# Kernel tuning notes

Hardware: AMD Instinct MI355X
Metric: run time of the kernel (lower is better)

The kernel has to match this reference:

```python
import jax, jax.numpy as jnp
import numpy as np

B, N, T, F = 4, 5000, 16, 64
E = 80000
H, C_OUT = 4, 16           # attention heads, per-head out channels
S = H * C_OUT              # stream_dim = 64
HID = 192                  # encoder hidden_dim = 3 * S
NEG_SLOPE = 0.2
EPS_SM = 1e-16             # PyG softmax eps
EPS_LN = 1e-5


def setup_inputs() -> dict:
    key = jax.random.key(0)
    ks = jax.random.split(key, 12)
    rn = lambda k, shape, s=0.1: jax.random.normal(k, shape, jnp.float32) * s
    return {
        "x_seq": rn(ks[0], (T, B, N, F), 1.0),
        "lin_w": rn(ks[1], (3, S, F)),          # per-stream GAT linear [out,in]
        "att_src": rn(ks[2], (3, H, C_OUT)),
        "att_dst": rn(ks[3], (3, H, C_OUT)),
        "gat_bias": jnp.zeros((3, S), jnp.float32),
        "w_ih": rn(ks[4], (3, 4 * S, S)),       # LSTMCell input weights (i,f,g,o)
        "w_hh": rn(ks[5], (3, 4 * S, S)),
        "b_ih": jnp.zeros((3, 4 * S), jnp.float32),
        "b_hh": jnp.zeros((3, 4 * S), jnp.float32),
        "ln_g": jnp.ones((3, S), jnp.float32),
        "ln_b": jnp.zeros((3, S), jnp.float32),
        "attn_w1": rn(ks[6], (HID // 2, 3 * S)),
        "attn_b1": jnp.zeros((HID // 2,), jnp.float32),
        "attn_w2": rn(ks[7], (3, HID // 2)),
        "attn_b2": jnp.zeros((3,), jnp.float32),
        "edge_index": jax.random.randint(ks[8], (2, E), 0, N, jnp.int32),
    }


def _batched_edges(edge_index):
    # replicate the graph B times with node-id offsets, then add self loops
    offs = (jnp.arange(B, dtype=edge_index.dtype) * N)[:, None]
    src = (edge_index[0][None, :] + offs).reshape(-1)
    dst = (edge_index[1][None, :] + offs).reshape(-1)
    loops = jnp.arange(B * N, dtype=edge_index.dtype)
    return jnp.concatenate([src, loops]), jnp.concatenate([dst, loops])


def _gat(x, src, dst, lin_w, a_src, a_dst, bias):
    # x: [B,N,F] -> out: [B,N,S]
    xt = (x.reshape(B * N, F) @ lin_w.T).reshape(B * N, H, C_OUT)
    xj, xi = xt[src], xt[dst]                               # [Eb,H,C]
    a = jnp.einsum('ehc,hc->eh', xj, a_src) + jnp.einsum('ehc,hc->eh', xi, a_dst)
    a = jax.nn.leaky_relu(a, NEG_SLOPE)
    amax = jax.ops.segment_max(a, dst, num_segments=B * N)  # segment-softmax over target
    ex = jnp.exp(a - amax[dst])
    den = jax.ops.segment_sum(ex, dst, num_segments=B * N)
    alpha = ex / (den[dst] + EPS_SM)
    out = jax.ops.segment_sum(xj * alpha[..., None], dst, num_segments=B * N)
    return out.reshape(B, N, S) + bias


def _cell(x, h, c, src, dst, lin_w, a_s, a_d, gb, wih, whh, bih, bhh, g, b):
    # one TemporalGNNCell step; h,c: [B*N,S]
    sp = _gat(x, src, dst, lin_w, a_s, a_d, gb).reshape(B * N, S)
    gates = sp @ wih.T + bih + h @ whh.T + bhh
    i, f, gg, o = jnp.split(gates, 4, axis=-1)
    c_new = jax.nn.sigmoid(f) * c + jax.nn.sigmoid(i) * jnp.tanh(gg)
    h_new = jax.nn.sigmoid(o) * jnp.tanh(c_new)
    mu = h_new.mean(-1, keepdims=True)
    var = ((h_new - mu) ** 2).mean(-1, keepdims=True)
    h_ln = (h_new - mu) / jnp.sqrt(var + EPS_LN) * g + b
    return h_ln, c_new


def reference(x_seq, lin_w, att_src, att_dst, gat_bias, w_ih, w_hh, b_ih, b_hh,
              ln_g, ln_b, attn_w1, attn_b1, attn_w2, attn_b2, edge_index):
    src, dst = _batched_edges(edge_index)
    z = jnp.zeros((B * N, S), x_seq.dtype)
    hf = cf = hm = cm = hs = cs = z
    outs = []
    for t in range(T):
        x_t = x_seq[t]
        hf, cf = _cell(x_t, hf, cf, src, dst, lin_w[0], att_src[0], att_dst[0], gat_bias[0],
                       w_ih[0], w_hh[0], b_ih[0], b_hh[0], ln_g[0], ln_b[0])
        if t % 15 == 0:
            hm, cm = _cell(x_t, hm, cm, src, dst, lin_w[1], att_src[1], att_dst[1], gat_bias[1],
                           w_ih[1], w_hh[1], b_ih[1], b_hh[1], ln_g[1], ln_b[1])
        if t % 150 == 0:
            hs, cs = _cell(x_t, hs, cs, src, dst, lin_w[2], att_src[2], att_dst[2], gat_bias[2],
                           w_ih[2], w_hh[2], b_ih[2], b_hh[2], ln_g[2], ln_b[2])
        fast, med, slow = hf, hm, hs
        ms = jnp.concatenate([fast, med, slow], axis=-1)       # [B*N, 3S]
        w = jax.nn.softmax(jax.nn.relu(ms @ attn_w1.T + attn_b1) @ attn_w2.T + attn_b2, axis=-1)
        outs.append(w[:, 0:1] * fast + w[:, 1:2] * med + w[:, 2:3] * slow)
    # stack(dim=1) then permute(0,2,1,3): [B, N, T, S]
    out = jnp.stack(outs, 0).reshape(T, B, N, S).transpose(1, 2, 0, 3)
    return out
```

## Files before the change

### kernel.cpp

```cpp
#include <hip/hip_runtime.h>
#include <cstddef>

#define NNODES 20000
#define TT 16
#define EE 80000
#define BE 320000
#define EB 340000
#define NPER 5000

__device__ __forceinline__ float sigf(float x) { return 1.0f / (1.0f + __expf(-x)); }
__device__ __forceinline__ float lreluf(float x) { return x > 0.0f ? x : 0.2f * x; }

__global__ __launch_bounds__(256) void deg_count_k(const int* __restrict__ eidx, int* __restrict__ deg) {
  int e = blockIdx.x * 256 + threadIdx.x;
  if (e >= EB) return;
  int dst;
  if (e < BE) { int r = e % EE; int b = e / EE; dst = eidx[EE + r] + b * NPER; }
  else dst = e - BE;
  atomicAdd(&deg[dst], 1);
}

__global__ __launch_bounds__(1024) void scan_k(const int* __restrict__ deg, int* __restrict__ startp) {
  __shared__ int buf[1024];
  __shared__ int carry_s;
  int tid = threadIdx.x;
  if (tid == 0) carry_s = 0;
  __syncthreads();
  for (int base = 0; base < NNODES; base += 1024) {
    int i = base + tid;
    int v = (i < NNODES) ? deg[i] : 0;
    buf[tid] = v;
    __syncthreads();
    for (int off = 1; off < 1024; off <<= 1) {
      int tv = (tid >= off) ? buf[tid - off] : 0;
      __syncthreads();
      buf[tid] += tv;
      __syncthreads();
    }
    int incl = buf[tid];
    int carry = carry_s;
    if (i < NNODES) startp[i] = carry + incl - v;
    __syncthreads();
    if (tid == 1023) carry_s = carry + incl;
    __syncthreads();
  }
  if (tid == 0) startp[NNODES] = carry_s;
}

__global__ __launch_bounds__(256) void fill_k(const int* __restrict__ eidx, const int* __restrict__ startp,
                                              int* __restrict__ cnt, int* __restrict__ adj) {
  int e = blockIdx.x * 256 + threadIdx.x;
  if (e >= EB) return;
  int src, dst;
  if (e < BE) { int r = e % EE; int b = e / EE; src = eidx[r] + b * NPER; dst = eidx[EE + r] + b * NPER; }
  else { src = e - BE; dst = src; }
  int p = atomicAdd(&cnt[dst], 1);
  adj[startp[dst] + p] = src;
}

__global__ __launch_bounds__(256) void gemm_k64(
    const float* __restrict__ A0, const float* __restrict__ A1, const float* __restrict__ A2,
    const float* __restrict__ W0, const float* __restrict__ W1, const float* __restrict__ W2,
    int wld, int nseg, int M, int N,
    const float* __restrict__ bias0, const float* __restrict__ bias1,
    int relu, float* __restrict__ C, int cld,
    const float* __restrict__ attS, const float* __restrict__ attD,
    float* __restrict__ asrcOut, float* __restrict__ adstOut)
{
  __shared__ float As[16][132];
  __shared__ float Bs[16][68];
  const int tid = threadIdx.x;
  const int m0 = blockIdx.x * 128;
  const int n0 = blockIdx.y * 64;
  const int tr = tid >> 4;
  const int tc = tid & 15;
  float acc[8][4];
#pragma unroll
  for (int r = 0; r < 8; ++r)
#pragma unroll
    for (int c = 0; c < 4; ++c) acc[r][c] = 0.0f;

  const int lk = (tid & 3) * 4;
  const int lm = tid >> 2;

  for (int seg = 0; seg < nseg; ++seg) {
    const float* Ap = (seg == 0) ? A0 : ((seg == 1) ? A1 : A2);
    const float* Wp = (seg == 0) ? W0 : ((seg == 1) ? W1 : W2);
    for (int ko = 0; ko < 64; ko += 16) {
#pragma unroll
      for (int i = 0; i < 2; ++i) {
        int m = lm + i * 64;
        int gm = m0 + m;
        float4 v = make_float4(0.f, 0.f, 0.f, 0.f);
        if (gm < M) v = *reinterpret_cast<const float4*>(Ap + (size_t)gm * 64 + ko + lk);
        As[lk + 0][m] = v.x; As[lk + 1][m] = v.y; As[lk + 2][m] = v.z; As[lk + 3][m] = v.w;
      }
      {
        int gn = n0 + lm;
        float4 v = make_float4(0.f, 0.f, 0.f, 0.f);
        if (gn < N) v = *reinterpret_cast<const float4*>(Wp + (size_t)gn * wld + ko + lk);
        Bs[lk + 0][lm] = v.x; Bs[lk + 1][lm] = v.y; Bs[lk + 2][lm] = v.z; Bs[lk + 3][lm] = v.w;
      }
      __syncthreads();
#pragma unroll
      for (int k = 0; k < 16; ++k) {
        float4 a0 = *reinterpret_cast<const float4*>(&As[k][tr * 8]);
        float4 a1 = *reinterpret_cast<const float4*>(&As[k][tr * 8 + 4]);
        float4 bb = *reinterpret_cast<const float4*>(&Bs[k][tc * 4]);
        float av[8] = {a0.x, a0.y, a0.z, a0.w, a1.x, a1.y, a1.z, a1.w};
        float bv[4] = {bb.x, bb.y, bb.z, bb.w};
#pragma unroll
        for (int r = 0; r < 8; ++r)
#pragma unroll
          for (int c = 0; c < 4; ++c)
            acc[r][c] = fmaf(av[r], bv[c], acc[r][c]);
      }
      __syncthreads();
    }
  }

#pragma unroll
  for (int r = 0; r < 8; ++r) {
    int gm = m0 + tr * 8 + r;
    if (gm < M) {
#pragma unroll
      for (int c = 0; c < 4; ++c) {
        int gn = n0 + tc * 4 + c;
        if (gn < N) {
          float v = acc[r][c];
          if (bias0) v += bias0[gn];
          if (bias1) v += bias1[gn];
          if (relu) v = fmaxf(v, 0.0f);
          C[(size_t)gm * cld + gn] = v;
          acc[r][c] = v;
        }
      }
    }
  }

  if (attS != nullptr) {
    int g = tc >> 2;
    float s0 = attS[tc * 4 + 0], s1 = attS[tc * 4 + 1], s2 = attS[tc * 4 + 2], s3 = attS[tc * 4 + 3];
    float d0 = attD[tc * 4 + 0], d1 = attD[tc * 4 + 1], d2 = attD[tc * 4 + 2], d3 = attD[tc * 4 + 3];
#pragma unroll
    for (int r = 0; r < 8; ++r) {
      float ps = acc[r][0] * s0 + acc[r][1] * s1 + acc[r][2] * s2 + acc[r][3] * s3;
      float pd = acc[r][0] * d0 + acc[r][1] * d1 + acc[r][2] * d2 + acc[r][3] * d3;
      ps += __shfl_xor(ps, 1); ps += __shfl_xor(ps, 2);
      pd += __shfl_xor(pd, 1); pd += __shfl_xor(pd, 2);
      int gm = m0 + tr * 8 + r;
      if ((tc & 3) == 0 && gm < M) {
        asrcOut[gm * 4 + g] = ps;
        adstOut[gm * 4 + g] = pd;
      }
    }
  }
}

__global__ __launch_bounds__(256) void edge_gather_k(
    const int* __restrict__ startp, const int* __restrict__ adj,
    const float* __restrict__ asrc, const float* __restrict__ adst,
    const float* __restrict__ xt, const float* __restrict__ bias,
    float* __restrict__ sp)
{
  int node = blockIdx.x * 4 + (threadIdx.x >> 6);
  if (node >= NNODES) return;
  int lane = threadIdx.x & 63;
  int s0 = startp[node];
  int deg = startp[node + 1] - s0;

  float4 adv = *reinterpret_cast<const float4*>(adst + (size_t)node * 4);
  float ad0 = adv.x, ad1 = adv.y, ad2 = adv.z, ad3 = adv.w;

  float mx0 = -1e30f, mx1 = -1e30f, mx2 = -1e30f, mx3 = -1e30f;
  for (int e = lane; e < deg; e += 64) {
    int src = adj[s0 + e];
    float4 av = *reinterpret_cast<const float4*>(asrc + (size_t)src * 4);
    mx0 = fmaxf(mx0, lreluf(av.x + ad0));
    mx1 = fmaxf(mx1, lreluf(av.y + ad1));
    mx2 = fmaxf(mx2, lreluf(av.z + ad2));
    mx3 = fmaxf(mx3, lreluf(av.w + ad3));
  }
#pragma unroll
  for (int off = 1; off < 64; off <<= 1) {
    mx0 = fmaxf(mx0, __shfl_xor(mx0, off));
    mx1 = fmaxf(mx1, __shfl_xor(mx1, off));
    mx2 = fmaxf(mx2, __shfl_xor(mx2, off));
    mx3 = fmaxf(mx3, __shfl_xor(mx3, off));
  }
  float dn0 = 0.f, dn1 = 0.f, dn2 = 0.f, dn3 = 0.f;
  for (int e = lane; e < deg; e += 64) {
    int src = adj[s0 + e];
    float4 av = *reinterpret_cast<const float4*>(asrc + (size_t)src * 4);
    dn0 += __expf(lreluf(av.x + ad0) - mx0);
    dn1 += __expf(lreluf(av.y + ad1) - mx1);
    dn2 += __expf(lreluf(av.z + ad2) - mx2);
    dn3 += __expf(lreluf(av.w + ad3) - mx3);
  }
#pragma unroll
  for (int off = 1; off < 64; off <<= 1) {
    dn0 += __shfl_xor(dn0, off);
    dn1 += __shfl_xor(dn1, off);
    dn2 += __shfl_xor(dn2, off);
    dn3 += __shfl_xor(dn3, off);
  }
  int h = lane >> 4;
  float mxh = (h == 0) ? mx0 : (h == 1) ? mx1 : (h == 2) ? mx2 : mx3;
  float adh = (h == 0) ? ad0 : (h == 1) ? ad1 : (h == 2) ? ad2 : ad3;
  float dnh = (h == 0) ? dn0 : (h == 1) ? dn1 : (h == 2) ? dn2 : dn3;
  float rdh = 1.0f / (dnh + 1e-16f);

  float accv = 0.0f;
  for (int e = 0; e < deg; ++e) {
    int src = adj[s0 + e];
    float a = lreluf(asrc[src * 4 + h] + adh);
    float alpha = __expf(a - mxh) * rdh;
    accv = fmaf(alpha, xt[(size_t)src * 64 + lane], accv);
  }
  sp[(size_t)node * 64 + lane] = accv + bias[lane];
}

__global__ __launch_bounds__(256) void lstm_update_k(
    const float* __restrict__ gates, float* __restrict__ cst, float* __restrict__ hst,
    const float* __restrict__ g_ln, const float* __restrict__ b_ln)
{
  int node = blockIdx.x * 4 + (threadIdx.x >> 6);
  if (node >= NNODES) return;
  int lane = threadIdx.x & 63;
  size_t gb = (size_t)node * 256;
  float gi = gates[gb + lane];
  float gf = gates[gb + 64 + lane];
  float gg = gates[gb + 128 + lane];
  float go = gates[gb + 192 + lane];
  float c = cst[(size_t)node * 64 + lane];
  float cn = sigf(gf) * c + sigf(gi) * tanhf(gg);
  float hn = sigf(go) * tanhf(cn);

  float s = hn;
#pragma unroll
  for (int off = 1; off < 64; off <<= 1) s += __shfl_xor(s, off);
  float mu = s * (1.0f / 64.0f);
  float d = hn - mu;
  float v = d * d;
#pragma unroll
  for (int off = 1; off < 64; off <<= 1) v += __shfl_xor(v, off);
  float var = v * (1.0f / 64.0f);
  float hl = d * rsqrtf(var + 1e-5f) * g_ln[lane] + b_ln[lane];
  hst[(size_t)node * 64 + lane] = hl;
  cst[(size_t)node * 64 + lane] = cn;
}

__global__ __launch_bounds__(256) void mix_final_k(
    const float* __restrict__ hidden, const float* __restrict__ w2, const float* __restrict__ b2,
    const float* __restrict__ hf, const float* __restrict__ hm, const float* __restrict__ hs,
    float* __restrict__ out, int t)
{
  int node = blockIdx.x * 4 + (threadIdx.x >> 6);
  if (node >= NNODES) return;
  int lane = threadIdx.x & 63;
  size_t hb = (size_t)node * 96;
  float h0 = hidden[hb + lane];
  int j2 = 64 + (lane & 31);
  float h1 = hidden[hb + j2];
  if (lane >= 32) h1 = 0.0f;

  float p0 = w2[lane] * h0 + w2[j2] * h1;
  float p1 = w2[96 + lane] * h0 + w2[96 + j2] * h1;
  float p2 = w2[192 + lane] * h0 + w2[192 + j2] * h1;
#pragma unroll
  for (int off = 1; off < 64; off <<= 1) {
    p0 += __shfl_xor(p0, off);
    p1 += __shfl_xor(p1, off);
    p2 += __shfl_xor(p2, off);
  }
  float l0 = p0 + b2[0], l1 = p1 + b2[1], l2 = p2 + b2[2];
  float m = fmaxf(l0, fmaxf(l1, l2));
  float e0 = __expf(l0 - m), e1 = __expf(l1 - m), e2 = __expf(l2 - m);
  float rs = 1.0f / (e0 + e1 + e2);
  float w0 = e0 * rs, w1v = e1 * rs, w2v = e2 * rs;

  size_t nb = (size_t)node * 64 + lane;
  float o = w0 * hf[nb] + w1v * hm[nb] + w2v * hs[nb];
  out[((size_t)node * TT + t) * 64 + lane] = o;
}

static inline void run_cell(hipStream_t stream, int c,
    const float* xtp, float* hstate, float* cstate,
    const float* lin_w, const float* att_src, const float* att_dst, const float* gat_bias,
    const float* w_ih, const float* w_hh, const float* b_ih, const float* b_hh,
    const float* ln_g, const float* ln_b,
    float* xt, float* sp, float* gates, float* asrc, float* adst,
    const int* startp, const int* adj)
{
  gemm_k64<<<dim3(157, 1), 256, 0, stream>>>(
      xtp, nullptr, nullptr, lin_w + c * 4096, nullptr, nullptr, 64, 1, NNODES, 64,
      nullptr, nullptr, 0, xt, 64, att_src + c * 64, att_dst + c * 64, asrc, adst);
  edge_gather_k<<<5000, 256, 0, stream>>>(startp, adj, asrc, adst, xt, gat_bias + c * 64, sp);
  gemm_k64<<<dim3(157, 4), 256, 0, stream>>>(
      sp, hstate, nullptr, w_ih + c * 16384, w_hh + c * 16384, nullptr, 64, 2, NNODES, 256,
      b_ih + c * 256, b_hh + c * 256, 0, gates, 256, nullptr, nullptr, nullptr, nullptr);
  lstm_update_k<<<5000, 256, 0, stream>>>(gates, cstate, hstate, ln_g + c * 64, ln_b + c * 64);
}

extern "C" void kernel_launch(void* const* d_in, const int* in_sizes, int n_in,
                              void* d_out, int out_size, void* d_ws, size_t ws_size,
                              hipStream_t stream) {
  const float* x_seq   = (const float*)d_in[0];
  const float* lin_w   = (const float*)d_in[1];
  const float* att_src = (const float*)d_in[2];
  const float* att_dst = (const float*)d_in[3];
  const float* gat_bias= (const float*)d_in[4];
  const float* w_ih    = (const float*)d_in[5];
  const float* w_hh    = (const float*)d_in[6];
  const float* b_ih    = (const float*)d_in[7];
  const float* b_hh    = (const float*)d_in[8];
  const float* ln_g    = (const float*)d_in[9];
  const float* ln_b    = (const float*)d_in[10];
  const float* w1      = (const float*)d_in[11];
  const float* b1      = (const float*)d_in[12];
  const float* w2      = (const float*)d_in[13];
  const float* b2      = (const float*)d_in[14];
  const int*   eidx    = (const int*)d_in[15];
  float* out = (float*)d_out;

  float* fbase = (float*)d_ws;
  float* xt     = fbase;
  float* sp     = xt + 1280000;
  float* gates  = sp + 1280000;
  float* hidden = gates + 5120000;
  float* asrc   = hidden + 1920000;
  float* adst   = asrc + 80000;
  float* hf = adst + 80000;
  float* cf = hf + 1280000;
  float* hm = cf + 1280000;
  float* cm = hm + 1280000;
  float* hs = cm + 1280000;
  float* cs = hs + 1280000;
  int* deg    = (int*)(cs + 1280000);
  int* cnt    = deg + 20000;
  int* startp = cnt + 20000;
  int* adj    = startp + 20001;

  hipMemsetAsync(hf, 0, (size_t)6 * 1280000 * sizeof(float), stream);
  hipMemsetAsync(deg, 0, (size_t)40000 * sizeof(int), stream);

  deg_count_k<<<(EB + 255) / 256, 256, 0, stream>>>(eidx, deg);
  scan_k<<<1, 1024, 0, stream>>>(deg, startp);
  fill_k<<<(EB + 255) / 256, 256, 0, stream>>>(eidx, startp, cnt, adj);

  for (int t = 0; t < TT; ++t) {
    const float* xtp = x_seq + (size_t)t * NNODES * 64;
    run_cell(stream, 0, xtp, hf, cf, lin_w, att_src, att_dst, gat_bias,
             w_ih, w_hh, b_ih, b_hh, ln_g, ln_b, xt, sp, gates, asrc, adst, startp, adj);
    if (t % 15 == 0)
      run_cell(stream, 1, xtp, hm, cm, lin_w, att_src, att_dst, gat_bias,
               w_ih, w_hh, b_ih, b_hh, ln_g, ln_b, xt, sp, gates, asrc, adst, startp, adj);
    if (t == 0)
      run_cell(stream, 2, xtp, hs, cs, lin_w, att_src, att_dst, gat_bias,
               w_ih, w_hh, b_ih, b_hh, ln_g, ln_b, xt, sp, gates, asrc, adst, startp, adj);

    gemm_k64<<<dim3(157, 2), 256, 0, stream>>>(
        hf, hm, hs, w1, w1 + 64, w1 + 128, 192, 3, NNODES, 96,
        b1, nullptr, 1, hidden, 96, nullptr, nullptr, nullptr, nullptr);
    mix_final_k<<<5000, 256, 0, stream>>>(hidden, w2, b2, hf, hm, hs, out, t);
  }
}
```

Before: 2.562 ms.

## Use split-bf16 MFMA GEMMs and fuse gates GEMM with LSTM update

Replaces the FP32 SIMT tiled GEMMs with bf16 MFMA kernels. Each operand is split into high and low bf16 parts, and three MFMAs per tile keep accuracy close to FP32. The gate GEMM is fused with the LSTM/LayerNorm update so the gate buffer is never materialized. The attention-MLP GEMM is fused with the softmax mixing. Hidden states are stored as bf16 hi/lo pairs to feed the MFMAs directly, and weights are converted once per call. This removes the large gates/hidden intermediates and raises matrix throughput, at the cost of extra conversions and some precision risk.

```diff
diff --git a/kernel.cpp b/kernel.cpp
--- a/kernel.cpp
+++ b/kernel.cpp
@@ -1,15 +1,30 @@
 #include <hip/hip_runtime.h>
 #include <cstddef>
 
-#define NNODES 20000
+#define M_NODES 20000
 #define TT 16
 #define EE 80000
 #define BE 320000
 #define EB 340000
 #define NPER 5000
 
+typedef __attribute__((ext_vector_type(8))) short bf16x8;
+typedef __attribute__((ext_vector_type(4))) float f32x4;
+
 __device__ __forceinline__ float sigf(float x) { return 1.0f / (1.0f + __expf(-x)); }
 __device__ __forceinline__ float lreluf(float x) { return x > 0.0f ? x : 0.2f * x; }
+
+__device__ __forceinline__ unsigned short f2bf(float x) {
+  union { float f; unsigned u; } v; v.f = x;
+  unsigned r = v.u + 0x7FFF + ((v.u >> 16) & 1);
+  return (unsigned short)(r >> 16);
+}
+__device__ __forceinline__ float bf2f(unsigned short u) {
+  union { unsigned u; float f; } v; v.u = ((unsigned)u) << 16; return v.f;
+}
+__device__ __forceinline__ f32x4 mfma16(bf16x8 a, bf16x8 b, f32x4 c) {
+  return __builtin_amdgcn_mfma_f32_16x16x32_bf16(a, b, c, 0, 0, 0);
+}
 
 __global__ __launch_bounds__(256) void deg_count_k(const int* __restrict__ eidx, int* __restrict__ deg) {
   int e = blockIdx.x * 256 + threadIdx.x;
@@ -26,9 +41,9 @@
   int tid = threadIdx.x;
   if (tid == 0) carry_s = 0;
   __syncthreads();
-  for (int base = 0; base < NNODES; base += 1024) {
+  for (int base = 0; base < M_NODES; base += 1024) {
     int i = base + tid;
-    int v = (i < NNODES) ? deg[i] : 0;
+    int v = (i < M_NODES) ? deg[i] : 0;
     buf[tid] = v;
     __syncthreads();
     for (int off = 1; off < 1024; off <<= 1) {
@@ -39,12 +54,12 @@
     }
     int incl = buf[tid];
     int carry = carry_s;
-    if (i < NNODES) startp[i] = carry + incl - v;
+    if (i < M_NODES) startp[i] = carry + incl - v;
     __syncthreads();
     if (tid == 1023) carry_s = carry + incl;
     __syncthreads();
   }
-  if (tid == 0) startp[NNODES] = carry_s;
+  if (tid == 0) startp[M_NODES] = carry_s;
 }
 
 __global__ __launch_bounds__(256) void fill_k(const int* __restrict__ eidx, const int* __restrict__ startp,
@@ -58,113 +73,91 @@
   adj[startp[dst] + p] = src;
 }
 
-__global__ __launch_bounds__(256) void gemm_k64(
-    const float* __restrict__ A0, const float* __restrict__ A1, const float* __restrict__ A2,
-    const float* __restrict__ W0, const float* __restrict__ W1, const float* __restrict__ W2,
-    int wld, int nseg, int M, int N,
-    const float* __restrict__ bias0, const float* __restrict__ bias1,
-    int relu, float* __restrict__ C, int cld,
+__global__ __launch_bounds__(256) void convert_k(
+    const float* __restrict__ lin_w, const float* __restrict__ w_ih, const float* __restrict__ w_hh,
+    const float* __restrict__ w1, const float* __restrict__ b_ih, const float* __restrict__ b_hh,
+    unsigned short* __restrict__ linH, unsigned short* __restrict__ linL,
+    unsigned short* __restrict__ wihH, unsigned short* __restrict__ wihL,
+    unsigned short* __restrict__ whhH, unsigned short* __restrict__ whhL,
+    unsigned short* __restrict__ w1H, unsigned short* __restrict__ w1L,
+    float* __restrict__ bsum)
+{
+  int i = blockIdx.x * 256 + threadIdx.x;
+  if (i < 12288) { float w = lin_w[i]; unsigned short h = f2bf(w); linH[i] = h; linL[i] = f2bf(w - bf2f(h)); }
+  if (i < 49152) {
+    float w = w_ih[i]; unsigned short h = f2bf(w); wihH[i] = h; wihL[i] = f2bf(w - bf2f(h));
+    float v = w_hh[i]; unsigned short g = f2bf(v); whhH[i] = g; whhL[i] = f2bf(v - bf2f(g));
+  }
+  if (i < 18432) { float w = w1[i]; unsigned short h = f2bf(w); w1H[i] = h; w1L[i] = f2bf(w - bf2f(h)); }
+  if (i < 768) bsum[i] = b_ih[i] + b_hh[i];
+}
+
+__global__ __launch_bounds__(256) void xt_gemm_k(
+    const float* __restrict__ A, const unsigned short* __restrict__ WH, const unsigned short* __restrict__ WL,
     const float* __restrict__ attS, const float* __restrict__ attD,
-    float* __restrict__ asrcOut, float* __restrict__ adstOut)
+    float* __restrict__ xt, float* __restrict__ asrc, float* __restrict__ adst)
 {
-  __shared__ float As[16][132];
-  __shared__ float Bs[16][68];
-  const int tid = threadIdx.x;
-  const int m0 = blockIdx.x * 128;
-  const int n0 = blockIdx.y * 64;
-  const int tr = tid >> 4;
-  const int tc = tid & 15;
-  float acc[8][4];
-#pragma unroll
-  for (int r = 0; r < 8; ++r)
-#pragma unroll
-    for (int c = 0; c < 4; ++c) acc[r][c] = 0.0f;
-
-  const int lk = (tid & 3) * 4;
-  const int lm = tid >> 2;
-
-  for (int seg = 0; seg < nseg; ++seg) {
-    const float* Ap = (seg == 0) ? A0 : ((seg == 1) ? A1 : A2);
-    const float* Wp = (seg == 0) ? W0 : ((seg == 1) ? W1 : W2);
-    for (int ko = 0; ko < 64; ko += 16) {
-#pragma unroll
-      for (int i = 0; i < 2; ++i) {
-        int m = lm + i * 64;
-        int gm = m0 + m;
-        float4 v = make_float4(0.f, 0.f, 0.f, 0.f);
-        if (gm < M) v = *reinterpret_cast<const float4*>(Ap + (size_t)gm * 64 + ko + lk);
-        As[lk + 0][m] = v.x; As[lk + 1][m] = v.y; As[lk + 2][m] = v.z; As[lk + 3][m] = v.w;
+  const int lane = threadIdx.x & 63, wv = threadIdx.x >> 6;
+  const int l15 = lane & 15, lg = lane >> 4;
+  const int m0 = (blockIdx.x * 4 + wv) * 16;
+  int gm = m0 + l15; if (gm >= M_NODES) gm = M_NODES - 1;
+  const float* arow = A + (size_t)gm * 64;
+  bf16x8 aH[2], aL[2];
+#pragma unroll
+  for (int ch = 0; ch < 2; ++ch) {
+    float4 u0 = *reinterpret_cast<const float4*>(arow + ch * 32 + lg * 8);
+    float4 u1 = *reinterpret_cast<const float4*>(arow + ch * 32 + lg * 8 + 4);
+    float v[8] = {u0.x, u0.y, u0.z, u0.w, u1.x, u1.y, u1.z, u1.w};
+    bf16x8 th, tl;
+#pragma unroll
+    for (int i = 0; i < 8; ++i) {
+      unsigned short hi = f2bf(v[i]);
+      th[i] = (short)hi;
+      tl[i] = (short)f2bf(v[i] - bf2f(hi));
+    }
+    aH[ch] = th; aL[ch] = tl;
+  }
+  f32x4 acc[4];
+#pragma unroll
+  for (int nf = 0; nf < 4; ++nf) acc[nf] = (f32x4){0.f, 0.f, 0.f, 0.f};
+#pragma unroll
+  for (int nf = 0; nf < 4; ++nf) {
+#pragma unroll
+    for (int ch = 0; ch < 2; ++ch) {
+      size_t wo = (size_t)(nf * 16 + l15) * 64 + ch * 32 + lg * 8;
+      bf16x8 bH = *reinterpret_cast<const bf16x8*>(WH + wo);
+      bf16x8 bL = *reinterpret_cast<const bf16x8*>(WL + wo);
+      acc[nf] = mfma16(aH[ch], bH, acc[nf]);
+      acc[nf] = mfma16(aH[ch], bL, acc[nf]);
+      acc[nf] = mfma16(aL[ch], bH, acc[nf]);
+    }
+  }
+#pragma unroll
+  for (int nf = 0; nf < 4; ++nf) {
+    float sv = attS[nf * 16 + l15], dv = attD[nf * 16 + l15];
+#pragma unroll
+    for (int r = 0; r < 4; ++r) {
+      int row = m0 + lg * 4 + r;
+      float v = acc[nf][r];
+      float ps = v * sv, pd = v * dv;
+#pragma unroll
+      for (int off = 1; off < 16; off <<= 1) { ps += __shfl_xor(ps, off); pd += __shfl_xor(pd, off); }
+      if (row < M_NODES) {
+        xt[(size_t)row * 64 + nf * 16 + l15] = v;
+        if (l15 == 0) { asrc[row * 4 + nf] = ps; adst[row * 4 + nf] = pd; }
       }
-      {
-        int gn = n0 + lm;
-        float4 v = make_float4(0.f, 0.f, 0.f, 0.f);
-        if (gn < N) v = *reinterpret_cast<const float4*>(Wp + (size_t)gn * wld + ko + lk);
-        Bs[lk + 0][lm] = v.x; Bs[lk + 1][lm] = v.y; Bs[lk + 2][lm] = v.z; Bs[lk + 3][lm] = v.w;
-      }
-      __syncthreads();
-#pragma unroll
-      for (int k = 0; k < 16; ++k) {
-        float4 a0 = *reinterpret_cast<const float4*>(&As[k][tr * 8]);
-        float4 a1 = *reinterpret_cast<const float4*>(&As[k][tr * 8 + 4]);
-        float4 bb = *reinterpret_cast<const float4*>(&Bs[k][tc * 4]);
-        float av[8] = {a0.x, a0.y, a0.z, a0.w, a1.x, a1.y, a1.z, a1.w};
-        float bv[4] = {bb.x, bb.y, bb.z, bb.w};
-#pragma unroll
-        for (int r = 0; r < 8; ++r)
-#pragma unroll
-          for (int c = 0; c < 4; ++c)
-            acc[r][c] = fmaf(av[r], bv[c], acc[r][c]);
-      }
-      __syncthreads();
-    }
-  }
-
-#pragma unroll
-  for (int r = 0; r < 8; ++r) {
-    int gm = m0 + tr * 8 + r;
-    if (gm < M) {
-#pragma unroll
-      for (int c = 0; c < 4; ++c) {
-        int gn = n0 + tc * 4 + c;
-        if (gn < N) {
-          float v = acc[r][c];
-          if (bias0) v += bias0[gn];
-          if (bias1) v += bias1[gn];
-          if (relu) v = fmaxf(v, 0.0f);
-          C[(size_t)gm * cld + gn] = v;
-          acc[r][c] = v;
-        }
-      }
-    }
-  }
-
-  if (attS != nullptr) {
-    int g = tc >> 2;
-    float s0 = attS[tc * 4 + 0], s1 = attS[tc * 4 + 1], s2 = attS[tc * 4 + 2], s3 = attS[tc * 4 + 3];
-    float d0 = attD[tc * 4 + 0], d1 = attD[tc * 4 + 1], d2 = attD[tc * 4 + 2], d3 = attD[tc * 4 + 3];
-#pragma unroll
-    for (int r = 0; r < 8; ++r) {
-      float ps = acc[r][0] * s0 + acc[r][1] * s1 + acc[r][2] * s2 + acc[r][3] * s3;
-      float pd = acc[r][0] * d0 + acc[r][1] * d1 + acc[r][2] * d2 + acc[r][3] * d3;
-      ps += __shfl_xor(ps, 1); ps += __shfl_xor(ps, 2);
-      pd += __shfl_xor(pd, 1); pd += __shfl_xor(pd, 2);
-      int gm = m0 + tr * 8 + r;
-      if ((tc & 3) == 0 && gm < M) {
-        asrcOut[gm * 4 + g] = ps;
-        adstOut[gm * 4 + g] = pd;
-      }
-    }
-  }
-}
-
-__global__ __launch_bounds__(256) void edge_gather_k(
+    }
+  }
+}
+
+__global__ __launch_bounds__(256) void gather_k(
     const int* __restrict__ startp, const int* __restrict__ adj,
     const float* __restrict__ asrc, const float* __restrict__ adst,
     const float* __restrict__ xt, const float* __restrict__ bias,
-    float* __restrict__ sp)
+    unsigned short* __restrict__ spH, unsigned short* __restrict__ spL)
 {
   int node = blockIdx.x * 4 + (threadIdx.x >> 6);
-  if (node >= NNODES) return;
+  if (node >= M_NODES) return;
   int lane = threadIdx.x & 63;
   int s0 = startp[node];
   int deg = startp[node + 1] - s0;
@@ -217,151 +210,256 @@
     float alpha = __expf(a - mxh) * rdh;
     accv = fmaf(alpha, xt[(size_t)src * 64 + lane], accv);
   }
-  sp[(size_t)node * 64 + lane] = accv + bias[lane];
-}
-
-__global__ __launch_bounds__(256) void lstm_update_k(
-    const float* __restrict__ gates, float* __restrict__ cst, float* __restrict__ hst,
+  float v = accv + bias[lane];
+  unsigned short hi = f2bf(v);
+  spH[(size_t)node * 64 + lane] = hi;
+  spL[(size_t)node * 64 + lane] = f2bf(v - bf2f(hi));
+}
+
+__global__ __launch_bounds__(256) void gates_lstm_k(
+    const unsigned short* __restrict__ spH, const unsigned short* __restrict__ spL,
+    unsigned short* __restrict__ hH, unsigned short* __restrict__ hL,
+    const unsigned short* __restrict__ WihH, const unsigned short* __restrict__ WihL,
+    const unsigned short* __restrict__ WhhH, const unsigned short* __restrict__ WhhL,
+    const float* __restrict__ bsum, float* __restrict__ cst,
     const float* __restrict__ g_ln, const float* __restrict__ b_ln)
 {
-  int node = blockIdx.x * 4 + (threadIdx.x >> 6);
-  if (node >= NNODES) return;
-  int lane = threadIdx.x & 63;
-  size_t gb = (size_t)node * 256;
-  float gi = gates[gb + lane];
-  float gf = gates[gb + 64 + lane];
-  float gg = gates[gb + 128 + lane];
-  float go = gates[gb + 192 + lane];
-  float c = cst[(size_t)node * 64 + lane];
-  float cn = sigf(gf) * c + sigf(gi) * tanhf(gg);
-  float hn = sigf(go) * tanhf(cn);
-
-  float s = hn;
-#pragma unroll
-  for (int off = 1; off < 64; off <<= 1) s += __shfl_xor(s, off);
-  float mu = s * (1.0f / 64.0f);
-  float d = hn - mu;
-  float v = d * d;
-#pragma unroll
-  for (int off = 1; off < 64; off <<= 1) v += __shfl_xor(v, off);
-  float var = v * (1.0f / 64.0f);
-  float hl = d * rsqrtf(var + 1e-5f) * g_ln[lane] + b_ln[lane];
-  hst[(size_t)node * 64 + lane] = hl;
-  cst[(size_t)node * 64 + lane] = cn;
-}
-
-__global__ __launch_bounds__(256) void mix_final_k(
-    const float* __restrict__ hidden, const float* __restrict__ w2, const float* __restrict__ b2,
-    const float* __restrict__ hf, const float* __restrict__ hm, const float* __restrict__ hs,
+  const int lane = threadIdx.x & 63, wv = threadIdx.x >> 6;
+  const int l15 = lane & 15, lg = lane >> 4;
+  const int m0 = (blockIdx.x * 4 + wv) * 16;
+  int gm = m0 + l15; if (gm >= M_NODES) gm = M_NODES - 1;
+  bf16x8 sHa[2], sLa[2], hHa[2], hLa[2];
+#pragma unroll
+  for (int ch = 0; ch < 2; ++ch) {
+    size_t off = (size_t)gm * 64 + ch * 32 + lg * 8;
+    sHa[ch] = *reinterpret_cast<const bf16x8*>(spH + off);
+    sLa[ch] = *reinterpret_cast<const bf16x8*>(spL + off);
+    hHa[ch] = *reinterpret_cast<const bf16x8*>(hH + off);
+    hLa[ch] = *reinterpret_cast<const bf16x8*>(hL + off);
+  }
+  f32x4 acc[16];
+#pragma unroll
+  for (int nf = 0; nf < 16; ++nf) acc[nf] = (f32x4){0.f, 0.f, 0.f, 0.f};
+#pragma unroll
+  for (int nf = 0; nf < 16; ++nf) {
+#pragma unroll
+    for (int ch = 0; ch < 2; ++ch) {
+      size_t wo = (size_t)(nf * 16 + l15) * 64 + ch * 32 + lg * 8;
+      bf16x8 bH = *reinterpret_cast<const bf16x8*>(WihH + wo);
+      bf16x8 bL = *reinterpret_cast<const bf16x8*>(WihL + wo);
+      acc[nf] = mfma16(sHa[ch], bH, acc[nf]);
+      acc[nf] = mfma16(sHa[ch], bL, acc[nf]);
+      acc[nf] = mfma16(sLa[ch], bH, acc[nf]);
+      bf16x8 cH = *reinterpret_cast<const bf16x8*>(WhhH + wo);
+      bf16x8 cL = *reinterpret_cast<const bf16x8*>(WhhL + wo);
+      acc[nf] = mfma16(hHa[ch], cH, acc[nf]);
+      acc[nf] = mfma16(hHa[ch], cL, acc[nf]);
+      acc[nf] = mfma16(hLa[ch], cH, acc[nf]);
+    }
+  }
+  float hn[4][4], cn[4][4];
+#pragma unroll
+  for (int cq = 0; cq < 4; ++cq) {
+    int col = cq * 16 + l15;
+    float bi = bsum[col], bff = bsum[64 + col], bg = bsum[128 + col], bo = bsum[192 + col];
+#pragma unroll
+    for (int r = 0; r < 4; ++r) {
+      int row = m0 + lg * 4 + r;
+      int crow = (row < M_NODES) ? row : (M_NODES - 1);
+      float gi = acc[cq][r] + bi;
+      float gf = acc[cq + 4][r] + bff;
+      float gg = acc[cq + 8][r] + bg;
+      float go = acc[cq + 12][r] + bo;
+      float cold = cst[(size_t)crow * 64 + col];
+      float cv = sigf(gf) * cold + sigf(gi) * tanhf(gg);
+      float hv = sigf(go) * tanhf(cv);
+      cn[cq][r] = cv; hn[cq][r] = hv;
+    }
+  }
+#pragma unroll
+  for (int r = 0; r < 4; ++r) {
+    float s = hn[0][r] + hn[1][r] + hn[2][r] + hn[3][r];
+#pragma unroll
+    for (int off = 1; off < 16; off <<= 1) s += __shfl_xor(s, off);
+    float mu = s * (1.0f / 64.0f);
+    float vv = 0.f;
+#pragma unroll
+    for (int cq = 0; cq < 4; ++cq) { float d = hn[cq][r] - mu; vv += d * d; }
+#pragma unroll
+    for (int off = 1; off < 16; off <<= 1) vv += __shfl_xor(vv, off);
+    float rstd = rsqrtf(vv * (1.0f / 64.0f) + 1e-5f);
+    int row = m0 + lg * 4 + r;
+    if (row < M_NODES) {
+#pragma unroll
+      for (int cq = 0; cq < 4; ++cq) {
+        int col = cq * 16 + l15;
+        float hl = (hn[cq][r] - mu) * rstd * g_ln[col] + b_ln[col];
+        unsigned short hi = f2bf(hl);
+        hH[(size_t)row * 64 + col] = hi;
+        hL[(size_t)row * 64 + col] = f2bf(hl - bf2f(hi));
+        cst[(size_t)row * 64 + col] = cn[cq][r];
+      }
+    }
+  }
+}
+
+__global__ __launch_bounds__(256) void mix_k(
+    const unsigned short* __restrict__ hHf, const unsigned short* __restrict__ hLf,
+    const unsigned short* __restrict__ hHm, const unsigned short* __restrict__ hLm,
+    const unsigned short* __restrict__ hHs, const unsigned short* __restrict__ hLs,
+    const unsigned short* __restrict__ W1H, const unsigned short* __restrict__ W1L,
+    const float* __restrict__ b1, const float* __restrict__ w2, const float* __restrict__ b2,
     float* __restrict__ out, int t)
 {
-  int node = blockIdx.x * 4 + (threadIdx.x >> 6);
-  if (node >= NNODES) return;
-  int lane = threadIdx.x & 63;
-  size_t hb = (size_t)node * 96;
-  float h0 = hidden[hb + lane];
-  int j2 = 64 + (lane & 31);
-  float h1 = hidden[hb + j2];
-  if (lane >= 32) h1 = 0.0f;
-
-  float p0 = w2[lane] * h0 + w2[j2] * h1;
-  float p1 = w2[96 + lane] * h0 + w2[96 + j2] * h1;
-  float p2 = w2[192 + lane] * h0 + w2[192 + j2] * h1;
-#pragma unroll
-  for (int off = 1; off < 64; off <<= 1) {
-    p0 += __shfl_xor(p0, off);
-    p1 += __shfl_xor(p1, off);
-    p2 += __shfl_xor(p2, off);
-  }
-  float l0 = p0 + b2[0], l1 = p1 + b2[1], l2 = p2 + b2[2];
-  float m = fmaxf(l0, fmaxf(l1, l2));
-  float e0 = __expf(l0 - m), e1 = __expf(l1 - m), e2 = __expf(l2 - m);
-  float rs = 1.0f / (e0 + e1 + e2);
-  float w0 = e0 * rs, w1v = e1 * rs, w2v = e2 * rs;
-
-  size_t nb = (size_t)node * 64 + lane;
-  float o = w0 * hf[nb] + w1v * hm[nb] + w2v * hs[nb];
-  out[((size_t)node * TT + t) * 64 + lane] = o;
-}
-
-static inline void run_cell(hipStream_t stream, int c,
-    const float* xtp, float* hstate, float* cstate,
-    const float* lin_w, const float* att_src, const float* att_dst, const float* gat_bias,
-    const float* w_ih, const float* w_hh, const float* b_ih, const float* b_hh,
-    const float* ln_g, const float* ln_b,
-    float* xt, float* sp, float* gates, float* asrc, float* adst,
-    const int* startp, const int* adj)
-{
-  gemm_k64<<<dim3(157, 1), 256, 0, stream>>>(
-      xtp, nullptr, nullptr, lin_w + c * 4096, nullptr, nullptr, 64, 1, NNODES, 64,
-      nullptr, nullptr, 0, xt, 64, att_src + c * 64, att_dst + c * 64, asrc, adst);
-  edge_gather_k<<<5000, 256, 0, stream>>>(startp, adj, asrc, adst, xt, gat_bias + c * 64, sp);
-  gemm_k64<<<dim3(157, 4), 256, 0, stream>>>(
-      sp, hstate, nullptr, w_ih + c * 16384, w_hh + c * 16384, nullptr, 64, 2, NNODES, 256,
-      b_ih + c * 256, b_hh + c * 256, 0, gates, 256, nullptr, nullptr, nullptr, nullptr);
-  lstm_update_k<<<5000, 256, 0, stream>>>(gates, cstate, hstate, ln_g + c * 64, ln_b + c * 64);
+  const int lane = threadIdx.x & 63, wv = threadIdx.x >> 6;
+  const int l15 = lane & 15, lg = lane >> 4;
+  const int m0 = (blockIdx.x * 4 + wv) * 16;
+  int gm = m0 + l15; if (gm >= M_NODES) gm = M_NODES - 1;
+  bf16x8 aH[3][2], aL[3][2];
+#pragma unroll
+  for (int ch = 0; ch < 2; ++ch) {
+    size_t off = (size_t)gm * 64 + ch * 32 + lg * 8;
+    aH[0][ch] = *reinterpret_cast<const bf16x8*>(hHf + off);
+    aL[0][ch] = *reinterpret_cast<const bf16x8*>(hLf + off);
+    aH[1][ch] = *reinterpret_cast<const bf16x8*>(hHm + off);
+    aL[1][ch] = *reinterpret_cast<const bf16x8*>(hLm + off);
+    aH[2][ch] = *reinterpret_cast<const bf16x8*>(hHs + off);
+    aL[2][ch] = *reinterpret_cast<const bf16x8*>(hLs + off);
+  }
+  f32x4 acc[6];
+#pragma unroll
+  for (int nf = 0; nf < 6; ++nf) acc[nf] = (f32x4){0.f, 0.f, 0.f, 0.f};
+#pragma unroll
+  for (int nf = 0; nf < 6; ++nf) {
+#pragma unroll
+    for (int s = 0; s < 3; ++s) {
+#pragma unroll
+      for (int ch = 0; ch < 2; ++ch) {
+        size_t wo = (size_t)(nf * 16 + l15) * 192 + s * 64 + ch * 32 + lg * 8;
+        bf16x8 bH = *reinterpret_cast<const bf16x8*>(W1H + wo);
+        bf16x8 bL = *reinterpret_cast<const bf16x8*>(W1L + wo);
+        acc[nf] = mfma16(aH[s][ch], bH, acc[nf]);
+        acc[nf] = mfma16(aH[s][ch], bL, acc[nf]);
+        acc[nf] = mfma16(aL[s][ch], bH, acc[nf]);
+      }
+    }
+  }
+#pragma unroll
+  for (int r = 0; r < 4; ++r) {
+    float p0 = 0.f, p1 = 0.f, p2 = 0.f;
+#pragma unroll
+    for (int nf = 0; nf < 6; ++nf) {
+      int n = nf * 16 + l15;
+      float hdv = fmaxf(acc[nf][r] + b1[n], 0.f);
+      p0 = fmaf(hdv, w2[n], p0);
+      p1 = fmaf(hdv, w2[96 + n], p1);
+      p2 = fmaf(hdv, w2[192 + n], p2);
+    }
+#pragma unroll
+    for (int off = 1; off < 16; off <<= 1) {
+      p0 += __shfl_xor(p0, off); p1 += __shfl_xor(p1, off); p2 += __shfl_xor(p2, off);
+    }
+    float q0 = p0 + b2[0], q1 = p1 + b2[1], q2 = p2 + b2[2];
+    float mx = fmaxf(q0, fmaxf(q1, q2));
+    float e0 = __expf(q0 - mx), e1 = __expf(q1 - mx), e2 = __expf(q2 - mx);
+    float rs = 1.0f / (e0 + e1 + e2);
+    float w0 = e0 * rs, w1v = e1 * rs, w2v = e2 * rs;
+    int row = m0 + lg * 4 + r;
+    if (row < M_NODES) {
+      size_t ob = ((size_t)row * TT + t) * 64;
+      size_t hb = (size_t)row * 64;
+#pragma unroll
+      for (int q = 0; q < 4; ++q) {
+        int col = l15 + 16 * q;
+        float vf = bf2f(hHf[hb + col]) + bf2f(hLf[hb + col]);
+        float vm = bf2f(hHm[hb + col]) + bf2f(hLm[hb + col]);
+        float vs = bf2f(hHs[hb + col]) + bf2f(hLs[hb + col]);
+        out[ob + col] = w0 * vf + w1v * vm + w2v * vs;
+      }
+    }
+  }
 }
 
 extern "C" void kernel_launch(void* const* d_in, const int* in_sizes, int n_in,
                               void* d_out, int out_size, void* d_ws, size_t ws_size,
                               hipStream_t stream) {
-  const float* x_seq   = (const float*)d_in[0];
-  const float* lin_w   = (const float*)d_in[1];
-  const float* att_src = (const float*)d_in[2];
-  const float* att_dst = (const float*)d_in[3];
-  const float* gat_bias= (const float*)d_in[4];
-  const float* w_ih    = (const float*)d_in[5];
-  const float* w_hh    = (const float*)d_in[6];
-  const float* b_ih    = (const float*)d_in[7];
-  const float* b_hh    = (const float*)d_in[8];
-  const float* ln_g    = (const float*)d_in[9];
-  const float* ln_b    = (const float*)d_in[10];
-  const float* w1      = (const float*)d_in[11];
-  const float* b1      = (const float*)d_in[12];
-  const float* w2      = (const float*)d_in[13];
-  const float* b2      = (const float*)d_in[14];
-  const int*   eidx    = (const int*)d_in[15];
+  const float* x_seq    = (const float*)d_in[0];
+  const float* lin_w    = (const float*)d_in[1];
+  const float* att_src  = (const float*)d_in[2];
+  const float* att_dst  = (const float*)d_in[3];
+  const float* gat_bias = (const float*)d_in[4];
+  const float* w_ih     = (const float*)d_in[5];
+  const float* w_hh     = (const float*)d_in[6];
+  const float* b_ih     = (const float*)d_in[7];
+  const float* b_hh     = (const float*)d_in[8];
+  const float* ln_g     = (const float*)d_in[9];
+  const float* ln_b     = (const float*)d_in[10];
+  const float* w1       = (const float*)d_in[11];
+  const float* b1       = (const float*)d_in[12];
+  const float* w2       = (const float*)d_in[13];
+  const float* b2       = (const float*)d_in[14];
+  const int*   eidx     = (const int*)d_in[15];
   float* out = (float*)d_out;
 
-  float* fbase = (float*)d_ws;
-  float* xt     = fbase;
-  float* sp     = xt + 1280000;
-  float* gates  = sp + 1280000;
-  float* hidden = gates + 5120000;
-  float* asrc   = hidden + 1920000;
-  float* adst   = asrc + 80000;
-  float* hf = adst + 80000;
-  float* cf = hf + 1280000;
-  float* hm = cf + 1280000;
-  float* cm = hm + 1280000;
-  float* hs = cm + 1280000;
-  float* cs = hs + 1280000;
-  int* deg    = (int*)(cs + 1280000);
-  int* cnt    = deg + 20000;
+  char* base = (char*)d_ws;
+  float* c_st = (float*)base;
+  unsigned short* hbuf = (unsigned short*)(c_st + 3840000);
+  int* deg = (int*)(hbuf + 7680000);
+  int* cnt = deg + 20000;
   int* startp = cnt + 20000;
-  int* adj    = startp + 20001;
-
-  hipMemsetAsync(hf, 0, (size_t)6 * 1280000 * sizeof(float), stream);
-  hipMemsetAsync(deg, 0, (size_t)40000 * sizeof(int), stream);
-
+  int* adj = startp + 20008;
+  float* asrc = (float*)(adj + 340000);
+  float* adst = asrc + 80000;
+  float* bsum = adst + 80000;
+  float* xt = bsum + 768;
+  unsigned short* spH = (unsigned short*)(xt + 1280000);
+  unsigned short* spL = spH + 1280000;
+  unsigned short* linH = spL + 1280000;
+  unsigned short* linL = linH + 12288;
+  unsigned short* wihH = linL + 12288;
+  unsigned short* wihL = wihH + 49152;
+  unsigned short* whhH = wihL + 49152;
+  unsigned short* whhL = whhH + 49152;
+  unsigned short* w1H = whhL + 49152;
+  unsigned short* w1L = w1H + 18432;
+
+  unsigned short* hHf = hbuf;
+  unsigned short* hLf = hbuf + 1280000;
+  unsigned short* hHm = hbuf + 2 * 1280000;
+  unsigned short* hLm = hbuf + 3 * 1280000;
+  unsigned short* hHs = hbuf + 4 * 1280000;
+  unsigned short* hLs = hbuf + 5 * 1280000;
+
+  hipMemsetAsync(base, 0, (size_t)3840000 * 4 + (size_t)7680000 * 2 + (size_t)40000 * 4, stream);
+
+  convert_k<<<192, 256, 0, stream>>>(lin_w, w_ih, w_hh, w1, b_ih, b_hh,
+                                     linH, linL, wihH, wihL, whhH, whhL, w1H, w1L, bsum);
   deg_count_k<<<(EB + 255) / 256, 256, 0, stream>>>(eidx, deg);
   scan_k<<<1, 1024, 0, stream>>>(deg, startp);
   fill_k<<<(EB + 255) / 256, 256, 0, stream>>>(eidx, startp, cnt, adj);
 
   for (int t = 0; t < TT; ++t) {
-    const float* xtp = x_seq + (size_t)t * NNODES * 64;
-    run_cell(stream, 0, xtp, hf, cf, lin_w, att_src, att_dst, gat_bias,
-             w_ih, w_hh, b_ih, b_hh, ln_g, ln_b, xt, sp, gates, asrc, adst, startp, adj);
-    if (t % 15 == 0)
-      run_cell(stream, 1, xtp, hm, cm, lin_w, att_src, att_dst, gat_bias,
-               w_ih, w_hh, b_ih, b_hh, ln_g, ln_b, xt, sp, gates, asrc, adst, startp, adj);
-    if (t == 0)
-      run_cell(stream, 2, xtp, hs, cs, lin_w, att_src, att_dst, gat_bias,
-               w_ih, w_hh, b_ih, b_hh, ln_g, ln_b, xt, sp, gates, asrc, adst, startp, adj);
-
-    gemm_k64<<<dim3(157, 2), 256, 0, stream>>>(
-        hf, hm, hs, w1, w1 + 64, w1 + 128, 192, 3, NNODES, 96,
-        b1, nullptr, 1, hidden, 96, nullptr, nullptr, nullptr, nullptr);
-    mix_final_k<<<5000, 256, 0, stream>>>(hidden, w2, b2, hf, hm, hs, out, t);
-  }
-}
+    const float* xtp = x_seq + (size_t)t * 1280000;
+    xt_gemm_k<<<313, 256, 0, stream>>>(xtp, linH, linL, att_src, att_dst, xt, asrc, adst);
+    gather_k<<<5000, 256, 0, stream>>>(startp, adj, asrc, adst, xt, gat_bias, spH, spL);
+    gates_lstm_k<<<313, 256, 0, stream>>>(spH, spL, hHf, hLf, wihH, wihL, whhH, whhL,
+                                          bsum, c_st, ln_g, ln_b);
+    if (t % 15 == 0) {
+      xt_gemm_k<<<313, 256, 0, stream>>>(xtp, linH + 4096, linL + 4096, att_src + 64, att_dst + 64,
+                                         xt, asrc, adst);
+      gather_k<<<5000, 256, 0, stream>>>(startp, adj, asrc, adst, xt, gat_bias + 64, spH, spL);
+      gates_lstm_k<<<313, 256, 0, stream>>>(spH, spL, hHm, hLm, wihH + 16384, wihL + 16384,
+                                            whhH + 16384, whhL + 16384, bsum + 256,
+                                            c_st + 1280000, ln_g + 64, ln_b + 64);
+    }
+    if (t == 0) {
+      xt_gemm_k<<<313, 256, 0, stream>>>(xtp, linH + 8192, linL + 8192, att_src + 128, att_dst + 128,
+                                         xt, asrc, adst);
+      gather_k<<<5000, 256, 0, stream>>>(startp, adj, asrc, adst, xt, gat_bias + 128, spH, spL);
+      gates_lstm_k<<<313, 256, 0, stream>>>(spH, spL, hHs, hLs, wihH + 32768, wihL + 32768,
+                                            whhH + 32768, whhL + 32768, bsum + 512,
+                                            c_st + 2560000, ln_g + 128, ln_b + 128);
+    }
+    mix_k<<<313, 256, 0, stream>>>(hHf, hLf, hHm, hLm, hHs, hLs, w1H, w1L, b1, w2, b2, out, t);
+  }
+}
```

Result: faster. 2.254 ms (-12.0%).
